# Kernel optimization log

Hardware: AMD Instinct MI355X
Metric: run time of the kernel (lower is better)

Reference implementation:

```python
import jax, jax.numpy as jnp
import numpy as np

GAMMA = 1.0 / 100.0  # _dtw_scaling_factor = 100 -> softmin temperature 1/100
BIG = 1e30           # finite stand-in for +inf (safe under logsumexp)
P = 2                # PairwiseDistance p


def _softmin3(a, b, c, gamma):
    # -gamma * log(exp(-a/g) + exp(-b/g) + exp(-c/g)), numerically stable
    z = jnp.stack([a, b, c]) * (-1.0 / gamma)
    return -gamma * jax.nn.logsumexp(z, axis=0)


def _softdtw_single(d, gamma):
    # d: [M, N] cost matrix; returns scalar R[M, N] of the soft-DTW recurrence
    # R[i, j] = d[i, j] + softmin(R[i-1, j-1], R[i-1, j], R[i, j-1])
    # with border R[0, 0] = 0, R[0, j>0] = R[i>0, 0] = +inf (padded formulation).
    M, N = d.shape
    init_prev = jnp.concatenate(
        [jnp.zeros((1,), d.dtype), jnp.full((N,), BIG, d.dtype)])  # R row -1 (padded, len N+1)

    def row_step(prev, d_row):
        def col_step(r_left, inputs):
            d_ij, r_diag, r_up = inputs
            r = d_ij + _softmin3(r_diag, r_up, r_left, gamma)
            return r, r
        _, row = jax.lax.scan(col_step, jnp.asarray(BIG, d.dtype),
                              (d_row, prev[:-1], prev[1:]))
        new_prev = jnp.concatenate([jnp.full((1,), BIG, d.dtype), row])
        return new_prev, None

    final_prev, _ = jax.lax.scan(row_step, init_prev, d)
    return final_prev[-1]


def setup_inputs() -> dict:
    key = jax.random.key(0)
    kx, ky = jax.random.split(key)
    x = jax.random.normal(kx, (64, 512), dtype=jnp.float32)
    y = jax.random.normal(ky, (64, 512), dtype=jnp.float32)
    return {"x": x, "y": y}


def reference(x, y):
    # D[b, i, j] = |x[b, j] - y[b, i]|^p  (matches PairwiseDistance)
    D = jnp.abs(x[:, None, :] - y[:, :, None]) ** P  # [B, M, N]
    return jax.vmap(lambda d: _softdtw_single(d, GAMMA))(D)  # [B]
```

## Files before the change

kernel.cpp:

```cpp
#include <hip/hip_runtime.h>


#define BIGF 1e30f
#define PADY 1e18f
#define SENTI 0x7fa00bad
#define INFBITS 0x7f800000u

__device__ __forceinline__ float dpp_shr1_old(float oldv, float v) {
    int o = __float_as_int(oldv);
    int i = __float_as_int(v);
    int r = __builtin_amdgcn_update_dpp(o, i, 0x138 , 0xF, 0xF, false);
    return __int_as_float(r);
}

__device__ __forceinline__ unsigned umax_(unsigned a, unsigned b) { return a > b ? a : b; }

__device__ __forceinline__ unsigned umax8f(float4 a, float4 b) {
    unsigned m0 = umax_(__float_as_uint(a.x), __float_as_uint(a.y));
    unsigned m1 = umax_(__float_as_uint(a.z), __float_as_uint(a.w));
    unsigned m2 = umax_(__float_as_uint(b.x), __float_as_uint(b.y));
    unsigned m3 = umax_(__float_as_uint(b.z), __float_as_uint(b.w));
    return umax_(umax_(m0, m1), umax_(m2, m3));
}

__global__ __launch_bounds__(256) void softdtw_kernel(
    const float* __restrict__ x, const float* __restrict__ y,
    float* __restrict__ out)
{
    constexpr int N = 512;
    const int b = blockIdx.x;
    const int tid = threadIdx.x;
    const int lane = tid & 63;
    const int wave = tid >> 6;

    __shared__ __align__(16) float ylds[1168];
    __shared__ __align__(16) float bnd[5][640];

    for (int k = tid; k < 640; k += 256) bnd[0][k] = BIGF;
    for (int k = tid; k < 2560; k += 256) ((int*)&bnd[1][0])[k] = SENTI;
    for (int k = tid; k < 1168; k += 256) {
        int i = k - 512;
        ylds[k] = ((unsigned)i < (unsigned)N) ? y[b * N + i] : PADY;
    }
    const int col0 = (wave << 7) + 2 * lane;
    const float x0 = x[b * N + col0];
    const float x1 = x[b * N + col0 + 1];
    __syncthreads();

    const float* srcb = &bnd[wave][0];
    float* dstb = &bnd[wave + 1][0];

    float r1a = BIGF, r1b = BIGF;
    float r2a = BIGF;
    float w7 = PADY;
    float c2, bcarry;
    float Ba[8], Bb[8];
#pragma unroll
    for (int k = 0; k < 8; ++k) Bb[k] = BIGF;

    {
        volatile const unsigned* sv = (volatile const unsigned*)srcb;
        unsigned a0, a1, b0, b1, b2, b3, b4, b5, b6, b7, mx;
        do {
            a0 = sv[15 * 8 + 6]; a1 = sv[15 * 8 + 7];
            b0 = sv[16 * 8 + 0]; b1 = sv[16 * 8 + 1];
            b2 = sv[16 * 8 + 2]; b3 = sv[16 * 8 + 3];
            b4 = sv[16 * 8 + 4]; b5 = sv[16 * 8 + 5];
            b6 = sv[16 * 8 + 6]; b7 = sv[16 * 8 + 7];
            unsigned c0 = sv[21 * 8 + 7];
            mx = umax_(umax_(umax_(a0, a1), umax_(b0, b1)),
                       umax_(umax_(b2, b3), umax_(b4, b5)));
            mx = umax_(mx, umax_(umax_(b6, b7), c0));
        } while (mx > INFBITS);
        c2     = __uint_as_float(a0);
        bcarry = __uint_as_float(a1);
        Ba[0] = __uint_as_float(b0); Ba[1] = __uint_as_float(b1);
        Ba[2] = __uint_as_float(b2); Ba[3] = __uint_as_float(b3);
        Ba[4] = __uint_as_float(b4); Ba[5] = __uint_as_float(b5);
        Ba[6] = __uint_as_float(b6); Ba[7] = __uint_as_float(b7);
        if (tid == 0) c2 = 0.0f;
    }

#define LOADW(W, idx) do { \
    const float2* p2_ = (const float2*)&ylds[idx]; \
    float2 a_ = p2_[0], b2_ = p2_[1], c_ = p2_[2], d2_ = p2_[3]; \
    W[0] = a_.x; W[1] = a_.y; W[2] = b2_.x; W[3] = b2_.y; \
    W[4] = c_.x; W[5] = c_.y; W[6] = d2_.x; W[7] = d2_.y; } while (0)

    float Wa[8], Wb[8];
    LOADW(Wa, 512 - 2 * lane);
    float bsv[8];

#define GSTEP(IT, WC, WN, BC, BN) do {                                       \
    const int it_ = (IT);                                                    \
    LOADW(WN, 512 - 2 * lane + 8 * (it_ + 1));     \
    const int Lp_ = it_ + 17;                \
    float4 qa_, qb_;                                                         \
    if (Lp_ <= 79) {                                                         \
        const float4* q_ = (const float4*)&srcb[Lp_ * 8];                    \
        qa_ = q_[0]; qb_ = q_[1];                                            \
    }                                                                        \
    _Pragma("unroll")                                                        \
    for (int t = 0; t < 8; ++t) {                  \
        const float oldv_ = t ? BC[t - 1] : bcarry;   \
        const float c1_ = dpp_shr1_old(oldv_, r1b);      \
        const float m0_ = fminf(fminf(c2, r1a), c1_);                        \
        const float d0_ = x0 - WC[t];                                        \
        const float v0_ = fmaf(d0_, d0_, m0_);                               \
        const float m1_ = fminf(fminf(r2a, r1b), r1a);                       \
        const float d1_ = x1 - (t ? WC[t - 1] : w7);                         \
        const float v1_ = fmaf(d1_, d1_, m1_);                               \
        bsv[t] = v1_;                                                        \
        r2a = r1a; r1a = v0_; r1b = v1_; c2 = c1_;                           \
    }                                                                        \
    if (lane == 63) {                   \
        float4* wf_ = (float4*)&dstb[it_ * 8];                               \
        wf_[0] = make_float4(bsv[0], bsv[1], bsv[2], bsv[3]);                \
        wf_[1] = make_float4(bsv[4], bsv[5], bsv[6], bsv[7]);                \
    }                                                                        \
    if (Lp_ <= 79) {                                                         \
        unsigned mx_ = umax8f(qa_, qb_);                                     \
        if (__builtin_expect(mx_ > INFBITS, 0)) {        \
            volatile const unsigned* pv_ = (volatile const unsigned*)&srcb[Lp_ * 8]; \
            unsigned u0_, u1_, u2_, u3_, u4_, u5_, u6_, u7_, m_;             \
            do {                                                             \
                u0_ = pv_[0]; u1_ = pv_[1]; u2_ = pv_[2]; u3_ = pv_[3];      \
                u4_ = pv_[4]; u5_ = pv_[5]; u6_ = pv_[6]; u7_ = pv_[7];      \
                m_ = umax_(umax_(umax_(u0_, u1_), umax_(u2_, u3_)),          \
                           umax_(umax_(u4_, u5_), umax_(u6_, u7_)));         \
            } while (m_ > INFBITS);                                          \
            qa_ = make_float4(__uint_as_float(u0_), __uint_as_float(u1_),    \
                              __uint_as_float(u2_), __uint_as_float(u3_));   \
            qb_ = make_float4(__uint_as_float(u4_), __uint_as_float(u5_),    \
                              __uint_as_float(u6_), __uint_as_float(u7_));   \
        }                                                                    \
        BN[0] = qa_.x; BN[1] = qa_.y; BN[2] = qa_.z; BN[3] = qa_.w;          \
        BN[4] = qb_.x; BN[5] = qb_.y; BN[6] = qb_.z; BN[7] = qb_.w;          \
    } else {                                \
        _Pragma("unroll")                                                    \
        for (int k = 0; k < 8; ++k) BN[k] = BIGF;                            \
    }                                                                        \
    bcarry = BC[7];                                                          \
    w7 = WC[7];                                                              \
} while (0)

    for (int it = 0; it < 80; it += 2) {
        GSTEP(it,     Wa, Wb, Ba, Bb);
        GSTEP(it + 1, Wb, Wa, Bb, Ba);
    }
#undef GSTEP
#undef LOADW

    if (tid == 255) out[b] = bsv[6];
}

extern "C" void kernel_launch(void* const* d_in, const int* in_sizes, int n_in,
                              void* d_out, int out_size, void* d_ws, size_t ws_size,
                              hipStream_t stream) {
    const float* x = (const float*)d_in[0];
    const float* y = (const float*)d_in[1];
    float* out = (float*)d_out;
    softdtw_kernel<<<64, 256, 0, stream>>>(x, y, out);
}
```

Measured before the change: 90.58 us.

## Double the per-step anti-diagonal chunk to 16 and align y loads via dual LDS copies

Each step now processes 16 anti-diagonals instead of 8, halving the number of outer iterations and inter-wave boundary handoffs (polls, lane-63 stores, sentinel checks). A second shifted copy of y in LDS lets odd and even lanes issue 16-byte aligned float4 loads instead of float2 loads. The cost is more registers for the wider W/B arrays, a longer startup wait before downstream waves can begin, and extra LDS for the duplicate y buffer.

```diff
diff --git a/kernel.cpp b/kernel.cpp
--- a/kernel.cpp
+++ b/kernel.cpp
@@ -15,12 +15,9 @@
 
 __device__ __forceinline__ unsigned umax_(unsigned a, unsigned b) { return a > b ? a : b; }
 
-__device__ __forceinline__ unsigned umax8f(float4 a, float4 b) {
-    unsigned m0 = umax_(__float_as_uint(a.x), __float_as_uint(a.y));
-    unsigned m1 = umax_(__float_as_uint(a.z), __float_as_uint(a.w));
-    unsigned m2 = umax_(__float_as_uint(b.x), __float_as_uint(b.y));
-    unsigned m3 = umax_(__float_as_uint(b.z), __float_as_uint(b.w));
-    return umax_(umax_(m0, m1), umax_(m2, m3));
+__device__ __forceinline__ unsigned umax4f(float4 a) {
+    return umax_(umax_(__float_as_uint(a.x), __float_as_uint(a.y)),
+                 umax_(__float_as_uint(a.z), __float_as_uint(a.w)));
 }
 
 __global__ __launch_bounds__(256) void softdtw_kernel(
@@ -33,14 +30,16 @@
     const int lane = tid & 63;
     const int wave = tid >> 6;
 
-    __shared__ __align__(16) float ylds[1168];
+    __shared__ __align__(16) float yldsA[1168];
+    __shared__ __align__(16) float yldsB[1168];
     __shared__ __align__(16) float bnd[5][640];
 
     for (int k = tid; k < 640; k += 256) bnd[0][k] = BIGF;
     for (int k = tid; k < 2560; k += 256) ((int*)&bnd[1][0])[k] = SENTI;
     for (int k = tid; k < 1168; k += 256) {
-        int i = k - 512;
-        ylds[k] = ((unsigned)i < (unsigned)N) ? y[b * N + i] : PADY;
+        int ia = k - 512, ib = k - 510;
+        yldsA[k] = ((unsigned)ia < (unsigned)N) ? y[b * N + ia] : PADY;
+        yldsB[k] = ((unsigned)ib < (unsigned)N) ? y[b * N + ib] : PADY;
     }
     const int col0 = (wave << 7) + 2 * lane;
     const float x0 = x[b * N + col0];
@@ -49,109 +48,119 @@
 
     const float* srcb = &bnd[wave][0];
     float* dstb = &bnd[wave + 1][0];
+    const float* ywp = (lane & 1) ? &yldsB[510 - 2 * lane] : &yldsA[512 - 2 * lane];
 
     float r1a = BIGF, r1b = BIGF;
     float r2a = BIGF;
-    float w7 = PADY;
+    float w15 = PADY;
     float c2, bcarry;
-    float Ba[8], Bb[8];
+    float Ba[16], Bb[16];
 #pragma unroll
-    for (int k = 0; k < 8; ++k) Bb[k] = BIGF;
+    for (int k = 0; k < 16; ++k) Bb[k] = BIGF;
 
     {
         volatile const unsigned* sv = (volatile const unsigned*)srcb;
-        unsigned a0, a1, b0, b1, b2, b3, b4, b5, b6, b7, mx;
+        unsigned s0, s1, g[16], mx;
         do {
-            a0 = sv[15 * 8 + 6]; a1 = sv[15 * 8 + 7];
-            b0 = sv[16 * 8 + 0]; b1 = sv[16 * 8 + 1];
-            b2 = sv[16 * 8 + 2]; b3 = sv[16 * 8 + 3];
-            b4 = sv[16 * 8 + 4]; b5 = sv[16 * 8 + 5];
-            b6 = sv[16 * 8 + 6]; b7 = sv[16 * 8 + 7];
-            unsigned c0 = sv[21 * 8 + 7];
-            mx = umax_(umax_(umax_(a0, a1), umax_(b0, b1)),
-                       umax_(umax_(b2, b3), umax_(b4, b5)));
-            mx = umax_(mx, umax_(umax_(b6, b7), c0));
+            s0 = sv[7 * 16 + 14]; s1 = sv[7 * 16 + 15];
+#pragma unroll
+            for (int j = 0; j < 16; ++j) g[j] = sv[8 * 16 + j];
+            unsigned mk = sv[11 * 16 + 15];
+            mx = umax_(umax_(s0, s1), mk);
+#pragma unroll
+            for (int j = 0; j < 16; ++j) mx = umax_(mx, g[j]);
         } while (mx > INFBITS);
-        c2     = __uint_as_float(a0);
-        bcarry = __uint_as_float(a1);
-        Ba[0] = __uint_as_float(b0); Ba[1] = __uint_as_float(b1);
-        Ba[2] = __uint_as_float(b2); Ba[3] = __uint_as_float(b3);
-        Ba[4] = __uint_as_float(b4); Ba[5] = __uint_as_float(b5);
-        Ba[6] = __uint_as_float(b6); Ba[7] = __uint_as_float(b7);
+        c2     = __uint_as_float(s0);
+        bcarry = __uint_as_float(s1);
+#pragma unroll
+        for (int j = 0; j < 16; ++j) Ba[j] = __uint_as_float(g[j]);
         if (tid == 0) c2 = 0.0f;
     }
 
-#define LOADW(W, idx) do { \
-    const float2* p2_ = (const float2*)&ylds[idx]; \
-    float2 a_ = p2_[0], b2_ = p2_[1], c_ = p2_[2], d2_ = p2_[3]; \
-    W[0] = a_.x; W[1] = a_.y; W[2] = b2_.x; W[3] = b2_.y; \
-    W[4] = c_.x; W[5] = c_.y; W[6] = d2_.x; W[7] = d2_.y; } while (0)
-
-    float Wa[8], Wb[8];
-    LOADW(Wa, 512 - 2 * lane);
-    float bsv[8];
+    float Wa[16], Wb[16];
+    {
+        const float4* p = (const float4*)&ywp[0];
+        float4 w0 = p[0], w1 = p[1], w2 = p[2], w3 = p[3];
+        Wa[0]=w0.x; Wa[1]=w0.y; Wa[2]=w0.z; Wa[3]=w0.w;
+        Wa[4]=w1.x; Wa[5]=w1.y; Wa[6]=w1.z; Wa[7]=w1.w;
+        Wa[8]=w2.x; Wa[9]=w2.y; Wa[10]=w2.z; Wa[11]=w2.w;
+        Wa[12]=w3.x; Wa[13]=w3.y; Wa[14]=w3.z; Wa[15]=w3.w;
+    }
+    float bsv[16];
 
 #define GSTEP(IT, WC, WN, BC, BN) do {                                       \
     const int it_ = (IT);                                                    \
-    LOADW(WN, 512 - 2 * lane + 8 * (it_ + 1));     \
-    const int Lp_ = it_ + 17;                \
-    float4 qa_, qb_;                                                         \
-    if (Lp_ <= 79) {                                                         \
-        const float4* q_ = (const float4*)&srcb[Lp_ * 8];                    \
-        qa_ = q_[0]; qb_ = q_[1];                                            \
+    {   const float4* p_ = (const float4*)&ywp[16 * (it_ + 1)];              \
+        float4 w0_ = p_[0], w1_ = p_[1], w2_ = p_[2], w3_ = p_[3];           \
+        WN[0]=w0_.x; WN[1]=w0_.y; WN[2]=w0_.z; WN[3]=w0_.w;                  \
+        WN[4]=w1_.x; WN[5]=w1_.y; WN[6]=w1_.z; WN[7]=w1_.w;                  \
+        WN[8]=w2_.x; WN[9]=w2_.y; WN[10]=w2_.z; WN[11]=w2_.w;                \
+        WN[12]=w3_.x; WN[13]=w3_.y; WN[14]=w3_.z; WN[15]=w3_.w; }            \
+    const int Lp_ = it_ + 9;                 \
+    float4 qa_, qb_, qc_, qd_;                                               \
+    if (Lp_ <= 39) {                                                         \
+        const float4* q_ = (const float4*)&srcb[Lp_ * 16];                   \
+        qa_ = q_[0]; qb_ = q_[1]; qc_ = q_[2]; qd_ = q_[3];                  \
     }                                                                        \
     _Pragma("unroll")                                                        \
-    for (int t = 0; t < 8; ++t) {                  \
+    for (int t = 0; t < 16; ++t) {                \
         const float oldv_ = t ? BC[t - 1] : bcarry;   \
         const float c1_ = dpp_shr1_old(oldv_, r1b);      \
         const float m0_ = fminf(fminf(c2, r1a), c1_);                        \
         const float d0_ = x0 - WC[t];                                        \
         const float v0_ = fmaf(d0_, d0_, m0_);                               \
         const float m1_ = fminf(fminf(r2a, r1b), r1a);                       \
-        const float d1_ = x1 - (t ? WC[t - 1] : w7);                         \
+        const float d1_ = x1 - (t ? WC[t - 1] : w15);                        \
         const float v1_ = fmaf(d1_, d1_, m1_);                               \
         bsv[t] = v1_;                                                        \
         r2a = r1a; r1a = v0_; r1b = v1_; c2 = c1_;                           \
     }                                                                        \
     if (lane == 63) {                   \
-        float4* wf_ = (float4*)&dstb[it_ * 8];                               \
-        wf_[0] = make_float4(bsv[0], bsv[1], bsv[2], bsv[3]);                \
-        wf_[1] = make_float4(bsv[4], bsv[5], bsv[6], bsv[7]);                \
+        float4* wf_ = (float4*)&dstb[it_ * 16];                              \
+        wf_[0] = make_float4(bsv[0],  bsv[1],  bsv[2],  bsv[3]);             \
+        wf_[1] = make_float4(bsv[4],  bsv[5],  bsv[6],  bsv[7]);             \
+        wf_[2] = make_float4(bsv[8],  bsv[9],  bsv[10], bsv[11]);            \
+        wf_[3] = make_float4(bsv[12], bsv[13], bsv[14], bsv[15]);            \
     }                                                                        \
-    if (Lp_ <= 79) {                                                         \
-        unsigned mx_ = umax8f(qa_, qb_);                                     \
+    if (Lp_ <= 39) {                                                         \
+        unsigned mx_ = umax_(umax_(umax4f(qa_), umax4f(qb_)),                \
+                             umax_(umax4f(qc_), umax4f(qd_)));               \
         if (__builtin_expect(mx_ > INFBITS, 0)) {        \
-            volatile const unsigned* pv_ = (volatile const unsigned*)&srcb[Lp_ * 8]; \
-            unsigned u0_, u1_, u2_, u3_, u4_, u5_, u6_, u7_, m_;             \
+            volatile const unsigned* pv_ = (volatile const unsigned*)&srcb[Lp_ * 16]; \
+            unsigned u_[16], m_;                                             \
             do {                                                             \
-                u0_ = pv_[0]; u1_ = pv_[1]; u2_ = pv_[2]; u3_ = pv_[3];      \
-                u4_ = pv_[4]; u5_ = pv_[5]; u6_ = pv_[6]; u7_ = pv_[7];      \
-                m_ = umax_(umax_(umax_(u0_, u1_), umax_(u2_, u3_)),          \
-                           umax_(umax_(u4_, u5_), umax_(u6_, u7_)));         \
+                m_ = 0u;                                                     \
+                _Pragma("unroll")                                            \
+                for (int j = 0; j < 16; ++j) { u_[j] = pv_[j]; m_ = umax_(m_, u_[j]); } \
             } while (m_ > INFBITS);                                          \
-            qa_ = make_float4(__uint_as_float(u0_), __uint_as_float(u1_),    \
-                              __uint_as_float(u2_), __uint_as_float(u3_));   \
-            qb_ = make_float4(__uint_as_float(u4_), __uint_as_float(u5_),    \
-                              __uint_as_float(u6_), __uint_as_float(u7_));   \
+            qa_ = make_float4(__uint_as_float(u_[0]),  __uint_as_float(u_[1]),  \
+                              __uint_as_float(u_[2]),  __uint_as_float(u_[3])); \
+            qb_ = make_float4(__uint_as_float(u_[4]),  __uint_as_float(u_[5]),  \
+                              __uint_as_float(u_[6]),  __uint_as_float(u_[7])); \
+            qc_ = make_float4(__uint_as_float(u_[8]),  __uint_as_float(u_[9]),  \
+                              __uint_as_float(u_[10]), __uint_as_float(u_[11])); \
+            qd_ = make_float4(__uint_as_float(u_[12]), __uint_as_float(u_[13]), \
+                              __uint_as_float(u_[14]), __uint_as_float(u_[15])); \
         }                                                                    \
-        BN[0] = qa_.x; BN[1] = qa_.y; BN[2] = qa_.z; BN[3] = qa_.w;          \
-        BN[4] = qb_.x; BN[5] = qb_.y; BN[6] = qb_.z; BN[7] = qb_.w;          \
+        BN[0]=qa_.x;  BN[1]=qa_.y;  BN[2]=qa_.z;  BN[3]=qa_.w;               \
+        BN[4]=qb_.x;  BN[5]=qb_.y;  BN[6]=qb_.z;  BN[7]=qb_.w;               \
+        BN[8]=qc_.x;  BN[9]=qc_.y;  BN[10]=qc_.z; BN[11]=qc_.w;              \
+        BN[12]=qd_.x; BN[13]=qd_.y; BN[14]=qd_.z; BN[15]=qd_.w;              \
     } else {                                \
         _Pragma("unroll")                                                    \
-        for (int k = 0; k < 8; ++k) BN[k] = BIGF;                            \
+        for (int k = 0; k < 16; ++k) BN[k] = BIGF;                           \
     }                                                                        \
-    bcarry = BC[7];                                                          \
-    w7 = WC[7];                                                              \
+    bcarry = BC[15];                                                         \
+    w15 = WC[15];                                                            \
 } while (0)
 
-    for (int it = 0; it < 80; it += 2) {
+    for (int it = 0; it < 40; it += 2) {
         GSTEP(it,     Wa, Wb, Ba, Bb);
         GSTEP(it + 1, Wb, Wa, Bb, Ba);
     }
 #undef GSTEP
-#undef LOADW
 
-    if (tid == 255) out[b] = bsv[6];
+    if (tid == 255) out[b] = bsv[14];
 }
 
 extern "C" void kernel_launch(void* const* d_in, const int* in_sizes, int n_in,
```

After: 85.74 us. -5.3%, faster.
